# Optimization experiments

Hardware: AMD Instinct MI355X
Metric: run time of the kernel (lower is better)

The kernel has to match this reference:

```python
import math
import jax, jax.numpy as jnp
import numpy as np

N_HEADS = 8

def setup_inputs() -> dict:
    key = jax.random.key(0)
    bs, n_heads, ch, l = 4, N_HEADS, 64, 1024
    width = 3 * n_heads * ch      # 1536 (packed q,k,v channels)
    T = 3 * l                     # 3072 (three spatial bands: ll, lh, hl)
    qkv = jax.random.normal(key, (bs, width, T), dtype=jnp.float32)
    return {"qkv": qkv, "l": l}

def reference(qkv, l):
    n_heads = N_HEADS
    bs, width, T = qkv.shape
    ch = width // (3 * n_heads)
    q, k, v = jnp.split(qkv, 3, axis=1)              # each (bs, n_heads*ch, T)
    scale = 1.0 / math.sqrt(math.sqrt(ch))
    qh = (q * scale).reshape(bs * n_heads, ch, T)
    kh = (k * scale).reshape(bs * n_heads, ch, T)
    vh = v.reshape(bs * n_heads, ch, T)
    # The original computes attention separately for q[:, :, :l], [l:2l], [2l:],
    # but k/v (and the softmax axis s) are identical, so computing attention
    # over the full query once and splitting the output is the same math.
    attn = jnp.einsum('bct,bcs->bts', qh, kh)        # (bs*H, T, T)
    w = jax.nn.softmax(attn.astype(jnp.float32), axis=-1).astype(attn.dtype)
    agg = jnp.einsum('bts,bcs->bct', w, vh).reshape(bs, n_heads * ch, T)
    return (agg[:, :, :l], agg[:, :, l:2 * l], agg[:, :, 2 * l:])
```

## Files before the change

kernel.cpp:

```cpp
#include <hip/hip_runtime.h>
#include <hip/hip_bf16.h>
#include <stdint.h>

#define T      3072
#define CH     64
#define HEADS  32
#define BM     128
#define BN     64
#define NIT    (T / BN)
#define PSTR   72

typedef unsigned short u16;
typedef short short8 __attribute__((ext_vector_type(8)));
typedef float floatx4 __attribute__((ext_vector_type(4)));

__device__ __forceinline__ unsigned pk2(float a, float b) {
  union { __hip_bfloat162 h; unsigned u; } cv;
  cv.h = __float22bfloat162_rn(float2{a, b});
  return cv.u;
}

__device__ __forceinline__ void gl_lds16(const void* g, void* l) {
  __builtin_amdgcn_global_load_lds(
      (const __attribute__((address_space(1))) uint32_t*)g,
      (__attribute__((address_space(3))) uint32_t*)l, 16, 0, 0);
}

__global__ __launch_bounds__(256) void qktrans(
    const float* __restrict__ qkv, u16* __restrict__ Qt, u16* __restrict__ Kt) {
  __shared__ __align__(16) u16 tl[64][PSTR];
  const int ttile = blockIdx.x, hh = blockIdx.y, role = blockIdx.z;
  const int b = hh >> 3, h = hh & 7;
  const int t0 = ttile * 64;
  const int tid = threadIdx.x;
  const float* src = qkv + (size_t)(b * 1536 + role * 512 + h * CH) * T;
  const float scale = (role == 0) ? 0.18033688011112042f : 1.0f;

#pragma unroll
  for (int p = 0; p < 2; ++p) {
    const int c0 = p * 32 + ((tid >> 4) << 1);
    const int ts = (tid & 15) * 4;
    float4 a = *(const float4*)(src + (size_t)c0 * T + t0 + ts);
    float4 c = *(const float4*)(src + (size_t)(c0 + 1) * T + t0 + ts);
    *(unsigned*)&tl[ts + 0][c0] = pk2(a.x * scale, c.x * scale);
    *(unsigned*)&tl[ts + 1][c0] = pk2(a.y * scale, c.y * scale);
    *(unsigned*)&tl[ts + 2][c0] = pk2(a.z * scale, c.z * scale);
    *(unsigned*)&tl[ts + 3][c0] = pk2(a.w * scale, c.w * scale);
  }
  __syncthreads();
  u16* dst = (role == 0 ? Qt : Kt) + (size_t)hh * T * CH;
#pragma unroll
  for (int q = 0; q < 2; ++q) {
    const int t = q * 32 + (tid >> 3);
    const int cc = (tid & 7) * 8;
    uint4 v = *(const uint4*)&tl[t][cc];
    *(uint4*)(dst + (size_t)(t0 + t) * CH + cc) = v;
  }
}

__global__ __launch_bounds__(256) void vcast(
    const float* __restrict__ qkv, u16* __restrict__ Vo) {
  const int b = blockIdx.y;
  const size_t i = ((size_t)blockIdx.x * 256 + threadIdx.x) * 8;
  const float4* s4 = (const float4*)(qkv + (size_t)b * 1536 * T + (size_t)1024 * T + i);
  float4 a = s4[0], c = s4[1];
  uint4 o;
  o.x = pk2(a.x, a.y); o.y = pk2(a.z, a.w);
  o.z = pk2(c.x, c.y); o.w = pk2(c.z, c.w);
  *(uint4*)(Vo + (size_t)b * 512 * T + i) = o;
}

__global__ __launch_bounds__(256, 3) void attn(
    const u16* __restrict__ Qt, const u16* __restrict__ Kt,
    const u16* __restrict__ Vg, float* __restrict__ out) {
  __shared__ __align__(16) u16 KB[2][BN * CH];
  __shared__ __align__(16) u16 VB[2][CH * BN];
  __shared__ __align__(16) u16 PL[4][32 * PSTR];

  const int qtile = blockIdx.x, hh = blockIdx.y;
  const int tid = threadIdx.x;
  const int wave = tid >> 6, lane = tid & 63;
  const int l15 = lane & 15, quad = lane >> 4;
  const int t0 = qtile * BM + wave * 32;

  const u16* Qh = Qt + (size_t)hh * T * CH;
  const u16* Kh = Kt + (size_t)hh * T * CH;
  const u16* Vh = Vg + (size_t)hh * CH * T;

  short8 qf[2][2];
#pragma unroll
  for (int tq = 0; tq < 2; ++tq)
#pragma unroll
    for (int kc = 0; kc < 2; ++kc)
      qf[tq][kc] = *(const short8*)(Qh + (size_t)(t0 + tq * 16 + l15) * CH + kc * 32 + quad * 8);

  floatx4 oacc[2][4] = {};
  float lsum[2][2] = {};

  int srow[2], scb[2];
#pragma unroll
  for (int j = 0; j < 2; ++j) {
    const int p = wave * 128 + j * 64 + lane;
    srow[j] = p >> 3;
    scb[j]  = (p & 7) ^ ((srow[j] + 2 * (srow[j] >> 3)) & 7);
  }
  const int swl = (l15 + 2 * (l15 >> 3)) & 7;
  u16* plw = PL[wave];

#define STAGE(buf, s0)                                                              \
  do {                                                                              \
    _Pragma("unroll")                                                               \
    for (int j = 0; j < 2; ++j)                                                     \
      gl_lds16(Kh + (size_t)((s0) + srow[j]) * CH + scb[j] * 8,                     \
               &KB[buf][(wave * 128 + j * 64) * 8]);                                \
    _Pragma("unroll")                                                               \
    for (int j = 0; j < 2; ++j)                                                     \
      gl_lds16(Vh + (size_t)srow[j] * T + (s0) + scb[j] * 8,                        \
               &VB[buf][(wave * 128 + j * 64) * 8]);                                \
  } while (0)

  STAGE(0, 0);

  for (int it = 0; it < NIT; ++it) {
    const int cur = it & 1;
    __syncthreads();
    if (it + 1 < NIT) STAGE(cur ^ 1, (it + 1) * BN);

    const u16* KL = KB[cur];
    const u16* VL = VB[cur];

    floatx4 sacc[2][4];
#pragma unroll
    for (int nt = 0; nt < 4; ++nt) {
      const int ph0 = quad ^ swl ^ ((nt & 1) * 4);
      const int base = (nt * 16 + l15) * CH;
      const short8 kf0 = *(const short8*)(KL + base + ph0 * 8);
      const short8 kf1 = *(const short8*)(KL + base + (ph0 ^ 4) * 8);
#pragma unroll
      for (int tq = 0; tq < 2; ++tq) {
        floatx4 z = {0.f, 0.f, 0.f, 0.f};
        z = __builtin_amdgcn_mfma_f32_16x16x32_bf16(kf0, qf[tq][0], z, 0, 0, 0);
        z = __builtin_amdgcn_mfma_f32_16x16x32_bf16(kf1, qf[tq][1], z, 0, 0, 0);
        sacc[tq][nt] = z;
      }
    }

#pragma unroll
    for (int tq = 0; tq < 2; ++tq)
#pragma unroll
      for (int nt = 0; nt < 4; ++nt) {
        floatx4 sv = sacc[tq][nt];
        float p0 = __builtin_amdgcn_exp2f(sv[0]);
        float p1 = __builtin_amdgcn_exp2f(sv[1]);
        float p2 = __builtin_amdgcn_exp2f(sv[2]);
        float p3 = __builtin_amdgcn_exp2f(sv[3]);
        lsum[tq][nt & 1] += (p0 + p1) + (p2 + p3);
        uint2 w; w.x = pk2(p0, p1); w.y = pk2(p2, p3);
        *(uint2*)(plw + (l15 + tq * 16) * PSTR + nt * 16 + quad * 4) = w;
      }

#pragma unroll
    for (int ks = 0; ks < 2; ++ks) {
      short8 pf0 = *(const short8*)(plw + l15 * PSTR + ks * 32 + quad * 8);
      short8 pf1 = *(const short8*)(plw + (l15 + 16) * PSTR + ks * 32 + quad * 8);
#pragma unroll
      for (int mt = 0; mt < 4; ++mt) {
        const int ph = quad ^ swl ^ ((mt & 1) * 4) ^ (ks * 4);
        const short8 vf = *(const short8*)(VL + (mt * 16 + l15) * BN + ph * 8);
        oacc[0][mt] = __builtin_amdgcn_mfma_f32_16x16x32_bf16(pf0, vf, oacc[0][mt], 0, 0, 0);
        oacc[1][mt] = __builtin_amdgcn_mfma_f32_16x16x32_bf16(pf1, vf, oacc[1][mt], 0, 0, 0);
      }
    }
  }

  float ls[2];
#pragma unroll
  for (int tq = 0; tq < 2; ++tq) {
    float s = lsum[tq][0] + lsum[tq][1];
    s += __shfl_xor(s, 16, 64);
    s += __shfl_xor(s, 32, 64);
    ls[tq] = s;
  }
  float linv[2][4];
#pragma unroll
  for (int tq = 0; tq < 2; ++tq)
#pragma unroll
    for (int r = 0; r < 4; ++r)
      linv[tq][r] = 1.0f / __shfl(ls[tq], quad * 4 + r, 64);

  const int b = hh >> 3, h = hh & 7;
#pragma unroll
  for (int tq = 0; tq < 2; ++tq) {
    const int tg = t0 + tq * 16 + quad * 4;
    const int band = tg >> 10, tt = tg & 1023;
    float* obase = out + (size_t)band * (4 * 512 * 1024)
                       + (size_t)b * (512 * 1024)
                       + (size_t)(h * CH) * 1024 + tt;
#pragma unroll
    for (int mt = 0; mt < 4; ++mt) {
      const int c = mt * 16 + l15;
      float4 v;
      v.x = oacc[tq][mt][0] * linv[tq][0];
      v.y = oacc[tq][mt][1] * linv[tq][1];
      v.z = oacc[tq][mt][2] * linv[tq][2];
      v.w = oacc[tq][mt][3] * linv[tq][3];
      *(float4*)(obase + (size_t)c * 1024) = v;
    }
  }
}

extern "C" void kernel_launch(void* const* d_in, const int* in_sizes, int n_in,
                              void* d_out, int out_size, void* d_ws, size_t ws_size,
                              hipStream_t stream) {
  (void)in_sizes; (void)n_in; (void)out_size; (void)ws_size;
  const float* qkv = (const float*)d_in[0];
  u16* Qt = (u16*)d_ws;
  u16* Kt = Qt + (size_t)HEADS * T * CH;
  u16* Vo = Kt + (size_t)HEADS * T * CH;
  float* out = (float*)d_out;

  qktrans<<<dim3(T / 64, HEADS, 2), 256, 0, stream>>>(qkv, Qt, Kt);
  vcast<<<dim3(768, 4), 256, 0, stream>>>(qkv, Vo);
  attn<<<dim3(T / BM, HEADS), 256, 0, stream>>>(Qt, Kt, Vo, out);
}
```

Before: 216.6 us.

## Merge K/V prep kernels, load Q directly in attention, keep K in registers

The separate K-transpose and V-cast kernels become one prep launch, and the Q transpose is dropped. The attention kernel now reads and scales Q from fp32 input directly with strided scalar loads. K tiles are no longer staged through LDS with async copies. Each wave loads the next K tile from global memory into registers right after the QK MFMAs. This removes one launch, the Q workspace round-trip and K LDS traffic, at the cost of redundant per-wave global K reads and more register pressure.

```diff
diff --git a/kernel.cpp b/kernel.cpp
--- a/kernel.cpp
+++ b/kernel.cpp
@@ -14,6 +14,8 @@
 typedef short short8 __attribute__((ext_vector_type(8)));
 typedef float floatx4 __attribute__((ext_vector_type(4)));
 
+#define QSCALE 0.18033688011112042f
+
 __device__ __forceinline__ unsigned pk2(float a, float b) {
   union { __hip_bfloat162 h; unsigned u; } cv;
   cv.h = __float22bfloat162_rn(float2{a, b});
@@ -26,15 +28,33 @@
       (__attribute__((address_space(3))) uint32_t*)l, 16, 0, 0);
 }
 
-__global__ __launch_bounds__(256) void qktrans(
-    const float* __restrict__ qkv, u16* __restrict__ Qt, u16* __restrict__ Kt) {
-  __shared__ __align__(16) u16 tl[64][PSTR];
-  const int ttile = blockIdx.x, hh = blockIdx.y, role = blockIdx.z;
+__global__ __launch_bounds__(256) void prep(
+    const float* __restrict__ qkv, u16* __restrict__ Kt, u16* __restrict__ Vo) {
+  const int tid = threadIdx.x;
+
+  if (blockIdx.z == 1) {
+    const int fb = blockIdx.x + 48 * blockIdx.y;
+    const int b = fb / 384, rem = fb - b * 384;
+    const size_t g = (size_t)rem * 4096 + tid * 16;
+    const float* src = qkv + (size_t)b * 1536 * T + (size_t)1024 * T + g;
+    uint4 o[2];
+#pragma unroll
+    for (int h = 0; h < 2; ++h) {
+      float4 a = *(const float4*)(src + h * 8);
+      float4 c = *(const float4*)(src + h * 8 + 4);
+      o[h].x = pk2(a.x, a.y); o[h].y = pk2(a.z, a.w);
+      o[h].z = pk2(c.x, c.y); o[h].w = pk2(c.z, c.w);
+    }
+    uint4* d = (uint4*)(Vo + (size_t)b * 512 * T + g);
+    d[0] = o[0]; d[1] = o[1];
+    return;
+  }
+
+  __shared__ u16 tl[64][66];
+  const int ttile = blockIdx.x, hh = blockIdx.y;
   const int b = hh >> 3, h = hh & 7;
   const int t0 = ttile * 64;
-  const int tid = threadIdx.x;
-  const float* src = qkv + (size_t)(b * 1536 + role * 512 + h * CH) * T;
-  const float scale = (role == 0) ? 0.18033688011112042f : 1.0f;
+  const float* src = qkv + (size_t)(b * 1536 + 512 + h * CH) * T;
 
 #pragma unroll
   for (int p = 0; p < 2; ++p) {
@@ -42,38 +62,29 @@
     const int ts = (tid & 15) * 4;
     float4 a = *(const float4*)(src + (size_t)c0 * T + t0 + ts);
     float4 c = *(const float4*)(src + (size_t)(c0 + 1) * T + t0 + ts);
-    *(unsigned*)&tl[ts + 0][c0] = pk2(a.x * scale, c.x * scale);
-    *(unsigned*)&tl[ts + 1][c0] = pk2(a.y * scale, c.y * scale);
-    *(unsigned*)&tl[ts + 2][c0] = pk2(a.z * scale, c.z * scale);
-    *(unsigned*)&tl[ts + 3][c0] = pk2(a.w * scale, c.w * scale);
+    *(unsigned*)&tl[ts + 0][c0] = pk2(a.x, c.x);
+    *(unsigned*)&tl[ts + 1][c0] = pk2(a.y, c.y);
+    *(unsigned*)&tl[ts + 2][c0] = pk2(a.z, c.z);
+    *(unsigned*)&tl[ts + 3][c0] = pk2(a.w, c.w);
   }
   __syncthreads();
-  u16* dst = (role == 0 ? Qt : Kt) + (size_t)hh * T * CH;
+  u16* dst = Kt + (size_t)hh * T * CH;
 #pragma unroll
   for (int q = 0; q < 2; ++q) {
     const int t = q * 32 + (tid >> 3);
     const int cc = (tid & 7) * 8;
-    uint4 v = *(const uint4*)&tl[t][cc];
+    uint4 v;
+    v.x = *(const unsigned*)&tl[t][cc + 0];
+    v.y = *(const unsigned*)&tl[t][cc + 2];
+    v.z = *(const unsigned*)&tl[t][cc + 4];
+    v.w = *(const unsigned*)&tl[t][cc + 6];
     *(uint4*)(dst + (size_t)(t0 + t) * CH + cc) = v;
   }
 }
 
-__global__ __launch_bounds__(256) void vcast(
-    const float* __restrict__ qkv, u16* __restrict__ Vo) {
-  const int b = blockIdx.y;
-  const size_t i = ((size_t)blockIdx.x * 256 + threadIdx.x) * 8;
-  const float4* s4 = (const float4*)(qkv + (size_t)b * 1536 * T + (size_t)1024 * T + i);
-  float4 a = s4[0], c = s4[1];
-  uint4 o;
-  o.x = pk2(a.x, a.y); o.y = pk2(a.z, a.w);
-  o.z = pk2(c.x, c.y); o.w = pk2(c.z, c.w);
-  *(uint4*)(Vo + (size_t)b * 512 * T + i) = o;
-}
-
 __global__ __launch_bounds__(256, 3) void attn(
-    const u16* __restrict__ Qt, const u16* __restrict__ Kt,
+    const float* __restrict__ qkv, const u16* __restrict__ Kt,
     const u16* __restrict__ Vg, float* __restrict__ out) {
-  __shared__ __align__(16) u16 KB[2][BN * CH];
   __shared__ __align__(16) u16 VB[2][CH * BN];
   __shared__ __align__(16) u16 PL[4][32 * PSTR];
 
@@ -82,17 +93,28 @@
   const int wave = tid >> 6, lane = tid & 63;
   const int l15 = lane & 15, quad = lane >> 4;
   const int t0 = qtile * BM + wave * 32;
-
-  const u16* Qh = Qt + (size_t)hh * T * CH;
+  const int b = hh >> 3, h = hh & 7;
+
   const u16* Kh = Kt + (size_t)hh * T * CH;
   const u16* Vh = Vg + (size_t)hh * CH * T;
 
+  const float* qsrc = qkv + (size_t)(b * 1536 + h * CH) * T;
   short8 qf[2][2];
 #pragma unroll
   for (int tq = 0; tq < 2; ++tq)
 #pragma unroll
-    for (int kc = 0; kc < 2; ++kc)
-      qf[tq][kc] = *(const short8*)(Qh + (size_t)(t0 + tq * 16 + l15) * CH + kc * 32 + quad * 8);
+    for (int kc = 0; kc < 2; ++kc) {
+      const int t = t0 + tq * 16 + l15;
+      unsigned w[4];
+#pragma unroll
+      for (int j = 0; j < 4; ++j) {
+        const int c = kc * 32 + quad * 8 + 2 * j;
+        float a = qsrc[(size_t)c * T + t] * QSCALE;
+        float d = qsrc[(size_t)(c + 1) * T + t] * QSCALE;
+        w[j] = pk2(a, d);
+      }
+      qf[tq][kc] = *(const short8*)&w[0];
+    }
 
   floatx4 oacc[2][4] = {};
   float lsum[2][2] = {};
@@ -107,42 +129,46 @@
   const int swl = (l15 + 2 * (l15 >> 3)) & 7;
   u16* plw = PL[wave];
 
-#define STAGE(buf, s0)                                                              \
+#define STAGEV(buf, s0)                                                             \
   do {                                                                              \
-    _Pragma("unroll")                                                               \
-    for (int j = 0; j < 2; ++j)                                                     \
-      gl_lds16(Kh + (size_t)((s0) + srow[j]) * CH + scb[j] * 8,                     \
-               &KB[buf][(wave * 128 + j * 64) * 8]);                                \
     _Pragma("unroll")                                                               \
     for (int j = 0; j < 2; ++j)                                                     \
       gl_lds16(Vh + (size_t)srow[j] * T + (s0) + scb[j] * 8,                        \
                &VB[buf][(wave * 128 + j * 64) * 8]);                                \
   } while (0)
 
-  STAGE(0, 0);
+  STAGEV(0, 0);
+
+  short8 kreg[4][2];
+#pragma unroll
+  for (int nt = 0; nt < 4; ++nt)
+#pragma unroll
+    for (int kc = 0; kc < 2; ++kc)
+      kreg[nt][kc] = *(const short8*)(Kh + (size_t)(nt * 16 + l15) * CH + kc * 32 + quad * 8);
 
   for (int it = 0; it < NIT; ++it) {
     const int cur = it & 1;
     __syncthreads();
-    if (it + 1 < NIT) STAGE(cur ^ 1, (it + 1) * BN);
-
-    const u16* KL = KB[cur];
-    const u16* VL = VB[cur];
+    if (it + 1 < NIT) STAGEV(cur ^ 1, (it + 1) * BN);
 
     floatx4 sacc[2][4];
 #pragma unroll
-    for (int nt = 0; nt < 4; ++nt) {
-      const int ph0 = quad ^ swl ^ ((nt & 1) * 4);
-      const int base = (nt * 16 + l15) * CH;
-      const short8 kf0 = *(const short8*)(KL + base + ph0 * 8);
-      const short8 kf1 = *(const short8*)(KL + base + (ph0 ^ 4) * 8);
+    for (int nt = 0; nt < 4; ++nt)
 #pragma unroll
       for (int tq = 0; tq < 2; ++tq) {
         floatx4 z = {0.f, 0.f, 0.f, 0.f};
-        z = __builtin_amdgcn_mfma_f32_16x16x32_bf16(kf0, qf[tq][0], z, 0, 0, 0);
-        z = __builtin_amdgcn_mfma_f32_16x16x32_bf16(kf1, qf[tq][1], z, 0, 0, 0);
+        z = __builtin_amdgcn_mfma_f32_16x16x32_bf16(kreg[nt][0], qf[tq][0], z, 0, 0, 0);
+        z = __builtin_amdgcn_mfma_f32_16x16x32_bf16(kreg[nt][1], qf[tq][1], z, 0, 0, 0);
         sacc[tq][nt] = z;
       }
+
+    if (it + 1 < NIT) {
+      const u16* Kp = Kh + (size_t)((it + 1) * BN + l15) * CH + quad * 8;
+#pragma unroll
+      for (int nt = 0; nt < 4; ++nt)
+#pragma unroll
+        for (int kc = 0; kc < 2; ++kc)
+          kreg[nt][kc] = *(const short8*)(Kp + (size_t)nt * 16 * CH + kc * 32);
     }
 
 #pragma unroll
@@ -166,7 +192,7 @@
 #pragma unroll
       for (int mt = 0; mt < 4; ++mt) {
         const int ph = quad ^ swl ^ ((mt & 1) * 4) ^ (ks * 4);
-        const short8 vf = *(const short8*)(VL + (mt * 16 + l15) * BN + ph * 8);
+        const short8 vf = *(const short8*)(VB[cur] + (mt * 16 + l15) * BN + ph * 8);
         oacc[0][mt] = __builtin_amdgcn_mfma_f32_16x16x32_bf16(pf0, vf, oacc[0][mt], 0, 0, 0);
         oacc[1][mt] = __builtin_amdgcn_mfma_f32_16x16x32_bf16(pf1, vf, oacc[1][mt], 0, 0, 0);
       }
@@ -188,7 +214,6 @@
     for (int r = 0; r < 4; ++r)
       linv[tq][r] = 1.0f / __shfl(ls[tq], quad * 4 + r, 64);
 
-  const int b = hh >> 3, h = hh & 7;
 #pragma unroll
   for (int tq = 0; tq < 2; ++tq) {
     const int tg = t0 + tq * 16 + quad * 4;
@@ -214,12 +239,10 @@
                               hipStream_t stream) {
   (void)in_sizes; (void)n_in; (void)out_size; (void)ws_size;
   const float* qkv = (const float*)d_in[0];
-  u16* Qt = (u16*)d_ws;
-  u16* Kt = Qt + (size_t)HEADS * T * CH;
+  u16* Kt = (u16*)d_ws;
   u16* Vo = Kt + (size_t)HEADS * T * CH;
   float* out = (float*)d_out;
 
-  qktrans<<<dim3(T / 64, HEADS, 2), 256, 0, stream>>>(qkv, Qt, Kt);
-  vcast<<<dim3(768, 4), 256, 0, stream>>>(qkv, Vo);
-  attn<<<dim3(T / BM, HEADS), 256, 0, stream>>>(Qt, Kt, Vo, out);
-}
+  prep<<<dim3(48, HEADS, 2), 256, 0, stream>>>(qkv, Kt, Vo);
+  attn<<<dim3(T / BM, HEADS), 256, 0, stream>>>(qkv, Kt, Vo, out);
+}
```

New measurement: 275.1 us. +27.0%, slower.
